# Optimization experiments

Measured on AMD Instinct MI355X. Metric: run time of the kernel, lower is better.

The kernel has to match this reference:

```python
import jax, jax.numpy as jnp
import numpy as np

OUT_F, IN_F = 11008, 4096
B, S = 2, 2048


def setup_inputs() -> dict:
    key = jax.random.key(0)
    k1, k2, k3 = jax.random.split(key, 3)
    x = jax.random.normal(k1, (B, S, IN_F), dtype=jnp.float32)
    # int8-valued quantized weight stored in int32 carrier, range [-128, 127]
    weight_q = jax.random.randint(k2, (OUT_F, IN_F), 0, 255, dtype=jnp.int32) - 128
    # realistic per-tensor quant params: small positive scale, zero_point near 0
    scale = jnp.float32(0.01)
    zero_point = jnp.float32(3.0)
    return {"x": x, "weight_q": weight_q, "scale": scale, "zero_point": zero_point}


def reference(x, weight_q, scale, zero_point):
    # Dequantize: w = scale * (q - zero_point)  -> [out_f, in_f] float32
    w = scale * (weight_q.astype(jnp.float32) - zero_point)
    # F.linear(x, w) = x @ w.T  -> [B, S, out_f]
    return jnp.einsum('bsi,oi->bso', x, w)
```

## Files before the change

### kernel.cpp

```cpp
#include <hip/hip_runtime.h>


#define M_DIM 4096
#define N_DIM 11008
#define K_DIM 4096
#define KT8 32
#define NT_N 43
#define NT_M 16

typedef __attribute__((ext_vector_type(4))) int i32x4;
typedef __attribute__((ext_vector_type(16))) int i32x16;
typedef __attribute__((ext_vector_type(4))) float f32x4;

__device__ inline unsigned short f2bf(float f) {
  unsigned int u = __float_as_uint(f);
  u += 0x7FFFu + ((u >> 16) & 1u);
  return (unsigned short)(u >> 16);
}

__global__ __launch_bounds__(256) void cvt_w_i8(const int* __restrict__ q,
                                                int4* __restrict__ wb, int n16) {
  int stride = gridDim.x * blockDim.x;
  for (int i = blockIdx.x * blockDim.x + threadIdx.x; i < n16; i += stride) {
    const int4* s = (const int4*)q + (size_t)i * 4;
    int4 a = s[0], b = s[1], c = s[2], d = s[3];
    int4 o;
    o.x = (a.x & 0xff) | ((a.y & 0xff) << 8) | ((a.z & 0xff) << 16) | ((a.w & 0xff) << 24);
    o.y = (b.x & 0xff) | ((b.y & 0xff) << 8) | ((b.z & 0xff) << 16) | ((b.w & 0xff) << 24);
    o.z = (c.x & 0xff) | ((c.y & 0xff) << 8) | ((c.z & 0xff) << 16) | ((c.w & 0xff) << 24);
    o.w = (d.x & 0xff) | ((d.y & 0xff) << 8) | ((d.z & 0xff) << 16) | ((d.w & 0xff) << 24);
    wb[i] = o;
  }
}

__global__ __launch_bounds__(256) void cvt_x_i8(const float* __restrict__ x,
                                                int4* __restrict__ xb,
                                                float* __restrict__ sx,
                                                float* __restrict__ rs) {
  const int row = blockIdx.x;
  const float* xr = x + (size_t)row * K_DIM;
  const int t = threadIdx.x;
  float4 v[4];
  float amax = 0.f, sum = 0.f;
#pragma unroll
  for (int j = 0; j < 4; ++j) {
    v[j] = *(const float4*)(xr + t * 16 + j * 4);
    amax = fmaxf(amax, fmaxf(fmaxf(fabsf(v[j].x), fabsf(v[j].y)),
                             fmaxf(fabsf(v[j].z), fabsf(v[j].w))));
    sum += (v[j].x + v[j].y) + (v[j].z + v[j].w);
  }
#pragma unroll
  for (int off = 1; off < 64; off <<= 1) {
    amax = fmaxf(amax, __shfl_xor(amax, off, 64));
    sum += __shfl_xor(sum, off, 64);
  }
  __shared__ float smx[4], sms[4];
  const int wv = t >> 6, ln = t & 63;
  if (ln == 0) { smx[wv] = amax; sms[wv] = sum; }
  __syncthreads();
  const float gmax = fmaxf(fmaxf(smx[0], smx[1]), fmaxf(smx[2], smx[3]));
  const float gsum = (sms[0] + sms[1]) + (sms[2] + sms[3]);
  const float gm = fmaxf(gmax, 1e-30f);
  const float qs = 127.f / gm;
  int b[16];
#pragma unroll
  for (int j = 0; j < 4; ++j) {
    b[j * 4 + 0] = (int)rintf(v[j].x * qs);
    b[j * 4 + 1] = (int)rintf(v[j].y * qs);
    b[j * 4 + 2] = (int)rintf(v[j].z * qs);
    b[j * 4 + 3] = (int)rintf(v[j].w * qs);
  }
  int4 o;
  o.x = (b[0] & 0xff) | ((b[1] & 0xff) << 8) | ((b[2] & 0xff) << 16) | ((b[3] & 0xff) << 24);
  o.y = (b[4] & 0xff) | ((b[5] & 0xff) << 8) | ((b[6] & 0xff) << 16) | ((b[7] & 0xff) << 24);
  o.z = (b[8] & 0xff) | ((b[9] & 0xff) << 8) | ((b[10] & 0xff) << 16) | ((b[11] & 0xff) << 24);
  o.w = (b[12] & 0xff) | ((b[13] & 0xff) << 8) | ((b[14] & 0xff) << 16) | ((b[15] & 0xff) << 24);
  xb[((size_t)row * K_DIM >> 4) + t] = o;
  if (t == 0) { sx[row] = gm / 127.f; rs[row] = gsum; }
}


__device__ __forceinline__ void stage_half(const char* __restrict__ gsrc,
                                           char* ldsBase, int w, int lane) {
  const int rsub = lane >> 3;
  const int csw  = ((lane & 7) ^ rsub) << 4;
#pragma unroll
  for (int r = 0; r < 2; ++r) {
    __builtin_amdgcn_global_load_lds(
        (const __attribute__((address_space(1))) void*)(
            gsrc + (size_t)(r * 64 + w * 8 + rsub) * K_DIM + csw),
        (__attribute__((address_space(3))) void*)(ldsBase + r * 8192 + w * 1024),
        16, 0, 0);
  }
}

#define DS_A32(d, mh)                                                               \
  do {                                                                              \
    _Pragma("unroll") for (int mi = 0; mi < 2; ++mi) {                              \
      _Pragma("unroll") for (int ks = 0; ks < 4; ++ks) {                            \
        a_frag[mi][ks] = *(const i32x4*)(ldsB + (d) * 65536 + aHalf + aRow +        \
                                         ((mh) * 2 + mi) * 4096 + kc32[ks]);        \
      }                                                                             \
    }                                                                               \
  } while (0)

#define DS_B32(d)                                                                   \
  do {                                                                              \
    _Pragma("unroll") for (int ni = 0; ni < 2; ++ni) {                              \
      _Pragma("unroll") for (int ks = 0; ks < 4; ++ks) {                            \
        b_frag[ni][ks] = *(const i32x4*)(ldsB + (d) * 65536 + bHalf + bRow +        \
                                         ni * 4096 + kc32[ks]);                     \
      }                                                                             \
    }                                                                               \
  } while (0)

#define MFMA32(mh)                                                                  \
  do {                                                                              \
    _Pragma("unroll") for (int mi = 0; mi < 2; ++mi) {                              \
      _Pragma("unroll") for (int ni = 0; ni < 2; ++ni) {                            \
        _Pragma("unroll") for (int ks = 0; ks < 4; ++ks) {                          \
          acc[(mh) * 2 + mi][ni] = __builtin_amdgcn_mfma_i32_32x32x32_i8(           \
              a_frag[mi][ks], b_frag[ni][ks], acc[(mh) * 2 + mi][ni], 0, 0, 0);     \
        }                                                                           \
      }                                                                             \
    }                                                                               \
  } while (0)

#define LGKM0_FENCE()                                                               \
  do {                                                                              \
    asm volatile("s_waitcnt lgkmcnt(0)" ::: "memory");                              \
    __builtin_amdgcn_sched_barrier(0);                                              \
  } while (0)

#define VMC4() asm volatile("s_waitcnt vmcnt(4)" ::: "memory")

__global__ __launch_bounds__(512, 2) void qgemm_i8(const char* __restrict__ Ai8,
                                                   const char* __restrict__ Wi8,
                                                   const float* __restrict__ sx,
                                                   const float* __restrict__ rs,
                                                   const float* __restrict__ sp,
                                                   const float* __restrict__ zpp,
                                                   float* __restrict__ C) {
  __shared__ char lds[131072];

  int bid = blockIdx.x;
  {
    const int cpx = (NT_M * NT_N) >> 3;
    bid = (bid & 7) * cpx + (bid >> 3);
  }
  const int mt = bid / NT_N;
  const int nt = bid % NT_N;

  const int tid  = threadIdx.x;
  const int w    = tid >> 6;
  const int lane = tid & 63;
  const int l31  = lane & 31;
  const int l5   = lane >> 5;
  const int wr   = w >> 2;
  const int wc   = w & 3;

  const char* gA = Ai8 + (size_t)(mt * 256) * K_DIM;
  const char* gB = Wi8 + (size_t)(nt * 256) * K_DIM;

  const char* ldsB = (const char*)lds;
  const unsigned aHalf = (unsigned)wr * 16384u;
  const unsigned bHalf = 32768u + (unsigned)(wc >> 1) * 16384u;
  const unsigned aRow  = (unsigned)l31 * 128u;
  const unsigned bRow  = (unsigned)((wc & 1) * 64 + l31) * 128u;
  const unsigned swz   = (unsigned)(lane & 7) << 4;
  const unsigned kc32[4] = {((unsigned)(0 * 32 + l5 * 16)) ^ swz,
                            ((unsigned)(1 * 32 + l5 * 16)) ^ swz,
                            ((unsigned)(2 * 32 + l5 * 16)) ^ swz,
                            ((unsigned)(3 * 32 + l5 * 16)) ^ swz};

  i32x4 a_frag[2][4];
  i32x4 b_frag[2][4];
  i32x16 acc[4][2];
#pragma unroll
  for (int m = 0; m < 4; ++m)
#pragma unroll
    for (int n = 0; n < 2; ++n) acc[m][n] = (i32x16)0;

  stage_half(gB, lds + 32768, w, lane);
  stage_half(gB + (size_t)128 * K_DIM, lds + 49152, w, lane);
  stage_half(gA, lds + 0, w, lane);
  stage_half(gA + (size_t)128 * K_DIM, lds + 16384, w, lane);
  stage_half(gB + 128, lds + 98304, w, lane);
  stage_half(gB + (size_t)128 * K_DIM + 128, lds + 114688, w, lane);
  VMC4();
  __builtin_amdgcn_s_barrier();

#pragma unroll 1
  for (int i = 0; i < KT8 / 2; ++i) {
    const int t1 = 2 * i + 1;
    const int c2 = (2 * i + 2 < KT8) ? 2 * i + 2 : KT8 - 1;
    const int c3 = (2 * i + 3 < KT8) ? 2 * i + 3 : KT8 - 1;

    DS_A32(0, 0);
    DS_B32(0);
    __builtin_amdgcn_s_barrier();
    stage_half(gA + (size_t)t1 * 128, lds + 65536, w, lane);
    stage_half(gA + (size_t)128 * K_DIM + (size_t)t1 * 128, lds + 81920, w, lane);
    LGKM0_FENCE();
    __builtin_amdgcn_s_setprio(1);
    MFMA32(0);
    __builtin_amdgcn_s_setprio(0);

    DS_A32(0, 1);
    __builtin_amdgcn_s_barrier();
    stage_half(gB + (size_t)c2 * 128, lds + 32768, w, lane);
    stage_half(gB + (size_t)128 * K_DIM + (size_t)c2 * 128, lds + 49152, w, lane);
    LGKM0_FENCE();
    __builtin_amdgcn_s_setprio(1);
    MFMA32(1);
    __builtin_amdgcn_s_setprio(0);
    VMC4();
    __builtin_amdgcn_s_barrier();

    DS_A32(1, 0);
    DS_B32(1);
    __builtin_amdgcn_s_barrier();
    stage_half(gA + (size_t)c2 * 128, lds + 0, w, lane);
    stage_half(gA + (size_t)128 * K_DIM + (size_t)c2 * 128, lds + 16384, w, lane);
    LGKM0_FENCE();
    __builtin_amdgcn_s_setprio(1);
    MFMA32(0);
    __builtin_amdgcn_s_setprio(0);

    DS_A32(1, 1);
    __builtin_amdgcn_s_barrier();
    stage_half(gB + (size_t)c3 * 128, lds + 98304, w, lane);
    stage_half(gB + (size_t)128 * K_DIM + (size_t)c3 * 128, lds + 114688, w, lane);
    LGKM0_FENCE();
    __builtin_amdgcn_s_setprio(1);
    MFMA32(1);
    __builtin_amdgcn_s_setprio(0);
    VMC4();
    __builtin_amdgcn_s_barrier();
  }

  const float s   = *sp;
  const float szp = s * (*zpp);
  const int grow0 = mt * 256 + wr * 128;
  const int gcol0 = nt * 256 + wc * 64 + l31;
#pragma unroll
  for (int ma = 0; ma < 4; ++ma) {
#pragma unroll
    for (int j = 0; j < 16; ++j) {
      const int m = grow0 + ma * 32 + (j & 3) + 8 * (j >> 2) + 4 * l5;
      const float alpha = s * sx[m];
      const float beta  = szp * rs[m];
#pragma unroll
      for (int ni = 0; ni < 2; ++ni)
        C[(size_t)m * N_DIM + (gcol0 + ni * 32)] =
            fmaf(alpha, (float)acc[ma][ni][j], -beta);
    }
  }
}


typedef __attribute__((ext_vector_type(8))) short short8_t;

__global__ __launch_bounds__(256) void qgemm_fused(const float* __restrict__ Ap,
                                                   const int* __restrict__ Bp,
                                                   const float* __restrict__ sp,
                                                   const float* __restrict__ zpp,
                                                   float* __restrict__ C) {
  __shared__ unsigned short As[128 * 64];
  __shared__ unsigned short Bs[128 * 64];
  int bid = blockIdx.x;
  {
    const int nwg = gridDim.x;
    if ((nwg & 7) == 0) bid = (bid & 7) * (nwg >> 3) + (bid >> 3);
  }
  const int mt = bid / (N_DIM / 128);
  const int nt = bid % (N_DIM / 128);
  const int tid = threadIdx.x, wave = tid >> 6, lane = tid & 63;
  const int l15 = lane & 15, l4 = lane >> 4, wr = wave >> 1, wcc = wave & 1;
  f32x4 acc[4][4];
#pragma unroll
  for (int m = 0; m < 4; ++m)
#pragma unroll
    for (int n = 0; n < 4; ++n) acc[m][n] = (f32x4)0.0f;
  const unsigned swz = (unsigned)(lane & 7) << 4;
  const unsigned aBase = (unsigned)(wr * 64 + l15) * 128;
  const unsigned bBase = (unsigned)(wcc * 64 + l15) * 128;
  const unsigned kc0 = ((unsigned)(l4 * 16)) ^ swz;
  const unsigned kc1 = ((unsigned)(64 + l4 * 16)) ^ swz;
  const char* AsB = (const char*)As;
  const char* BsB = (const char*)Bs;
  const float sc = *sp;
  const float nszp = -sc * (*zpp);
  for (int t = 0; t < K_DIM / 64; ++t) {
#pragma unroll
    for (int i = 0; i < 8; ++i) {
      const int c = i * 256 + tid;
      const int row = c >> 4, col = (c & 15) * 4;
      float4 v = *(const float4*)(Ap + (size_t)(mt * 128 + row) * K_DIM + t * 64 + col);
      ushort4 o = make_ushort4(f2bf(v.x), f2bf(v.y), f2bf(v.z), f2bf(v.w));
      const unsigned off = (unsigned)row * 128 +
                           (((unsigned)col * 2) ^ (((unsigned)(row & 7)) << 4));
      *(ushort4*)((char*)As + off) = o;
    }
#pragma unroll
    for (int i = 0; i < 8; ++i) {
      const int c = i * 256 + tid;
      const int row = c >> 4, col = (c & 15) * 4;
      int4 v = *(const int4*)(Bp + (size_t)(nt * 128 + row) * K_DIM + t * 64 + col);
      ushort4 o = make_ushort4(f2bf(fmaf(sc, (float)v.x, nszp)),
                               f2bf(fmaf(sc, (float)v.y, nszp)),
                               f2bf(fmaf(sc, (float)v.z, nszp)),
                               f2bf(fmaf(sc, (float)v.w, nszp)));
      const unsigned off = (unsigned)row * 128 +
                           (((unsigned)col * 2) ^ (((unsigned)(row & 7)) << 4));
      *(ushort4*)((char*)Bs + off) = o;
    }
    __syncthreads();
#pragma unroll
    for (int kk = 0; kk < 2; ++kk) {
      const unsigned kcx = kk ? kc1 : kc0;
      short8_t af[4], bfr[4];
#pragma unroll
      for (int m = 0; m < 4; ++m) af[m] = *(const short8_t*)(AsB + aBase + m * 2048 + kcx);
#pragma unroll
      for (int n = 0; n < 4; ++n) bfr[n] = *(const short8_t*)(BsB + bBase + n * 2048 + kcx);
#pragma unroll
      for (int m = 0; m < 4; ++m)
#pragma unroll
        for (int n = 0; n < 4; ++n)
          acc[m][n] = __builtin_amdgcn_mfma_f32_16x16x32_bf16(af[m], bfr[n], acc[m][n], 0, 0, 0);
    }
    __syncthreads();
  }
  const int grow = mt * 128 + wr * 64 + l4 * 4;
  const int gcol = nt * 128 + wcc * 64 + l15;
#pragma unroll
  for (int m = 0; m < 4; ++m)
#pragma unroll
    for (int n = 0; n < 4; ++n)
#pragma unroll
      for (int j = 0; j < 4; ++j)
        C[(size_t)(grow + m * 16 + j) * N_DIM + (gcol + n * 16)] = acc[m][n][j];
}

extern "C" void kernel_launch(void* const* d_in, const int* in_sizes, int n_in,
                              void* d_out, int out_size, void* d_ws, size_t ws_size,
                              hipStream_t stream) {
  const float* x   = (const float*)d_in[0];
  const int*   wq  = (const int*)d_in[1];
  const float* sp  = (const float*)d_in[2];
  const float* zpp = (const float*)d_in[3];
  float* out = (float*)d_out;

  const size_t wbytes = (size_t)N_DIM * K_DIM;
  const size_t xbytes = (size_t)M_DIM * K_DIM;
  const size_t need   = wbytes + xbytes + 2 * (size_t)M_DIM * sizeof(float);

  if (ws_size >= need) {
    char*  wb = (char*)d_ws;
    char*  xb = (char*)d_ws + wbytes;
    float* sx = (float*)((char*)d_ws + wbytes + xbytes);
    float* rs = sx + M_DIM;
    cvt_w_i8<<<2048, 256, 0, stream>>>(wq, (int4*)wb,
                                       (int)((size_t)N_DIM * K_DIM / 16));
    cvt_x_i8<<<M_DIM, 256, 0, stream>>>(x, (int4*)xb, sx, rs);
    qgemm_i8<<<NT_M * NT_N, 512, 0, stream>>>(xb, wb, sx, rs, sp, zpp, out);
  } else {
    qgemm_fused<<<(M_DIM / 128) * (N_DIM / 128), 256, 0, stream>>>(x, wq, sp, zpp, out);
  }
}
```

Baseline: 313.9 us.

## Change LDS swizzle to row-group XOR and drop explicit lgkmcnt fences

The LDS XOR swizzle key changes from the lane's low bits to the row index divided by four, modulo 8. It is applied consistently on the global_load_lds write side and on the ds_read fragment side, with the aim of cutting LDS bank conflicts for the 128-byte-row tiles. The explicit s_waitcnt lgkmcnt(0) plus sched_barrier fences before each MFMA block are removed, and barriers become inline-asm s_barrier. This lets the compiler interleave ds_reads with MFMAs. The risk is that the compiler's scheduling or waitcnt placement around the async LDS loads becomes less controlled.

```diff
diff --git a/kernel.cpp b/kernel.cpp
--- a/kernel.cpp
+++ b/kernel.cpp
@@ -83,7 +83,8 @@
 __device__ __forceinline__ void stage_half(const char* __restrict__ gsrc,
                                            char* ldsBase, int w, int lane) {
   const int rsub = lane >> 3;
-  const int csw  = ((lane & 7) ^ rsub) << 4;
+  const int g    = (2 * w + (rsub >> 2)) & 7;
+  const int csw  = ((lane & 7) ^ g) << 4;
 #pragma unroll
   for (int r = 0; r < 2; ++r) {
     __builtin_amdgcn_global_load_lds(
@@ -126,13 +127,8 @@
     }                                                                               \
   } while (0)
 
-#define LGKM0_FENCE()                                                               \
-  do {                                                                              \
-    asm volatile("s_waitcnt lgkmcnt(0)" ::: "memory");                              \
-    __builtin_amdgcn_sched_barrier(0);                                              \
-  } while (0)
-
-#define VMC4() asm volatile("s_waitcnt vmcnt(4)" ::: "memory")
+#define PHASE_BAR() asm volatile("s_barrier" ::: "memory")
+#define VMC4() asm volatile("s_waitcnt vmcnt(4)")
 
 __global__ __launch_bounds__(512, 2) void qgemm_i8(const char* __restrict__ Ai8,
                                                    const char* __restrict__ Wi8,
@@ -167,7 +163,7 @@
   const unsigned bHalf = 32768u + (unsigned)(wc >> 1) * 16384u;
   const unsigned aRow  = (unsigned)l31 * 128u;
   const unsigned bRow  = (unsigned)((wc & 1) * 64 + l31) * 128u;
-  const unsigned swz   = (unsigned)(lane & 7) << 4;
+  const unsigned swz   = (unsigned)((l31 >> 2) & 7) << 4;
   const unsigned kc32[4] = {((unsigned)(0 * 32 + l5 * 16)) ^ swz,
                             ((unsigned)(1 * 32 + l5 * 16)) ^ swz,
                             ((unsigned)(2 * 32 + l5 * 16)) ^ swz,
@@ -188,7 +184,7 @@
   stage_half(gB + 128, lds + 98304, w, lane);
   stage_half(gB + (size_t)128 * K_DIM + 128, lds + 114688, w, lane);
   VMC4();
-  __builtin_amdgcn_s_barrier();
+  PHASE_BAR();
 
 #pragma unroll 1
   for (int i = 0; i < KT8 / 2; ++i) {
@@ -198,45 +194,41 @@
 
     DS_A32(0, 0);
     DS_B32(0);
-    __builtin_amdgcn_s_barrier();
+    PHASE_BAR();
     stage_half(gA + (size_t)t1 * 128, lds + 65536, w, lane);
     stage_half(gA + (size_t)128 * K_DIM + (size_t)t1 * 128, lds + 81920, w, lane);
-    LGKM0_FENCE();
     __builtin_amdgcn_s_setprio(1);
     MFMA32(0);
     __builtin_amdgcn_s_setprio(0);
 
     DS_A32(0, 1);
-    __builtin_amdgcn_s_barrier();
+    PHASE_BAR();
     stage_half(gB + (size_t)c2 * 128, lds + 32768, w, lane);
     stage_half(gB + (size_t)128 * K_DIM + (size_t)c2 * 128, lds + 49152, w, lane);
-    LGKM0_FENCE();
     __builtin_amdgcn_s_setprio(1);
     MFMA32(1);
     __builtin_amdgcn_s_setprio(0);
     VMC4();
-    __builtin_amdgcn_s_barrier();
+    PHASE_BAR();
 
     DS_A32(1, 0);
     DS_B32(1);
-    __builtin_amdgcn_s_barrier();
+    PHASE_BAR();
     stage_half(gA + (size_t)c2 * 128, lds + 0, w, lane);
     stage_half(gA + (size_t)128 * K_DIM + (size_t)c2 * 128, lds + 16384, w, lane);
-    LGKM0_FENCE();
     __builtin_amdgcn_s_setprio(1);
     MFMA32(0);
     __builtin_amdgcn_s_setprio(0);
 
     DS_A32(1, 1);
-    __builtin_amdgcn_s_barrier();
+    PHASE_BAR();
     stage_half(gB + (size_t)c3 * 128, lds + 98304, w, lane);
     stage_half(gB + (size_t)128 * K_DIM + (size_t)c3 * 128, lds + 114688, w, lane);
-    LGKM0_FENCE();
     __builtin_amdgcn_s_setprio(1);
     MFMA32(1);
     __builtin_amdgcn_s_setprio(0);
     VMC4();
-    __builtin_amdgcn_s_barrier();
+    PHASE_BAR();
   }
 
   const float s   = *sp;
```

After: 304.1 us. -3.1%, faster.
